# Kernel tuning notes

Hardware: AMD Instinct MI355X
Metric: run time of the kernel (lower is better)

Reference implementation:

```python
import jax, jax.numpy as jnp
import numpy as np

B, S, D, H = 2, 2048, 1024, 16
DK = D // H  # 64
THETA = 10000.0


def _rope_tables(seq_len, d_k, theta):
    pos = jnp.arange(seq_len, dtype=jnp.float32)  # [S]
    dim = jnp.arange(0, d_k, 2, dtype=jnp.float32)  # [DK/2]
    inv_freq = 1.0 / theta ** (dim / d_k)
    angle = pos[:, None] * inv_freq[None, :]  # [S, DK/2]
    angle = jnp.repeat(angle, 2, axis=-1)  # repeat_interleave -> [S, DK]
    return jnp.cos(angle), jnp.sin(angle)


def _apply_rope(x, cos, sin):
    # x: [..., S, DK]; interleaved pair rotation
    x1 = x[..., ::2]
    x2 = x[..., 1::2]
    x_perm = jnp.stack([-x2, x1], axis=-1).reshape(x.shape)
    return x * cos + x_perm * sin


def setup_inputs() -> dict:
    key = jax.random.key(0)
    ks = jax.random.split(key, 5)
    std = np.sqrt(2.0 / (D + D)).astype(np.float32)
    return {
        "x": jax.random.normal(ks[0], (B, S, D), dtype=jnp.float32),
        "Wq": jax.random.normal(ks[1], (D, D), dtype=jnp.float32) * std,
        "Wk": jax.random.normal(ks[2], (D, D), dtype=jnp.float32) * std,
        "Wv": jax.random.normal(ks[3], (D, D), dtype=jnp.float32) * std,
        "Wo": jax.random.normal(ks[4], (D, D), dtype=jnp.float32) * std,
    }


def reference(x, Wq, Wk, Wv, Wo):
    seq_len = x.shape[-2]
    # projections: weight is [d_out, d_in], applied as x @ W^T
    def split_heads(t):
        return t.reshape(*t.shape[:-1], H, DK).swapaxes(-3, -2)  # [B, H, S, DK]

    Q = split_heads(jnp.einsum('bsd,od->bso', x, Wq))
    K = split_heads(jnp.einsum('bsd,od->bso', x, Wk))
    V = split_heads(jnp.einsum('bsd,od->bso', x, Wv))

    cos, sin = _rope_tables(seq_len, DK, THETA)  # [S, DK]
    Q = _apply_rope(Q, cos, sin)
    K = _apply_rope(K, cos, sin)

    scale = 1.0 / np.sqrt(DK).astype(np.float32)
    logits = jnp.einsum('bhnd,bhmd->bhnm', Q, K) * scale  # [B, H, S, S]
    causal = jnp.tril(jnp.ones((seq_len, seq_len), dtype=bool))
    logits = jnp.where(causal, logits, -jnp.inf)
    probs = jax.nn.softmax(logits, axis=-1)
    attn = jnp.einsum('bhnm,bhmd->bhnd', probs, V)  # [B, H, S, DK]
    attn = attn.swapaxes(-3, -2).reshape(*x.shape[:-1], D)  # [B, S, D]
    return jnp.einsum('bsd,od->bso', attn, Wo)
```

## Files before the change

### kernel.cpp

```cpp
#include <hip/hip_runtime.h>
#include <hip/hip_bf16.h>
#include <cstdint>
#include <cstddef>

#define BB 2
#define SS 2048
#define DD 1024
#define HH 16
#define DKK 64
#define MM (BB*SS)

typedef __bf16 bf16x8 __attribute__((ext_vector_type(8)));
typedef float  f32x4  __attribute__((ext_vector_type(4)));

__device__ __forceinline__ unsigned short f2bf(float f) {
    unsigned u = __float_as_uint(f);
    u += 0x7FFF + ((u >> 16) & 1);
    return (unsigned short)(u >> 16);
}

#if __has_builtin(__builtin_amdgcn_cvt_pk_bf16_f32)
typedef __bf16 bf16v2 __attribute__((ext_vector_type(2)));
__device__ __forceinline__ unsigned pk_bf16(float a, float b) {
    bf16v2 v = __builtin_amdgcn_cvt_pk_bf16_f32(a, b);
    return __builtin_bit_cast(unsigned, v);
}
#else
__device__ __forceinline__ unsigned pk_bf16(float a, float b) {
    return (unsigned)f2bf(a) | ((unsigned)f2bf(b) << 16);
}
#endif

__device__ __forceinline__ void gld_lds16(const void* g, void* l) {
    __builtin_amdgcn_global_load_lds(
        (const __attribute__((address_space(1))) unsigned int*)g,
        (__attribute__((address_space(3))) unsigned int*)l, 16, 0, 0);
}

#define WAIT_VM4() __builtin_amdgcn_s_waitcnt(0x0F74)
#define WAIT_VM3() __builtin_amdgcn_s_waitcnt(0x0F73)
#define WAIT_VM0() __builtin_amdgcn_s_waitcnt(0x0F70)
#define BARRIER()  __builtin_amdgcn_s_barrier()

__global__ __launch_bounds__(256) void cast_all(const float* __restrict__ x,
                                                const float* __restrict__ wq,
                                                const float* __restrict__ wk,
                                                const float* __restrict__ wv,
                                                const float* __restrict__ wo,
                                                unsigned short* __restrict__ xb,
                                                unsigned short* __restrict__ wb) {
    int i = (blockIdx.x * 256 + threadIdx.x) * 4;
    const float* src;
    unsigned short* dst;
    if (i < MM * DD) { src = x + i; dst = xb + i; }
    else {
        int e = i - MM * DD;
        int r = e >> 20;
        const float* s0 = (r == 0) ? wq : (r == 1) ? wk : (r == 2) ? wv : wo;
        src = s0 + (e & ((1 << 20) - 1));
        dst = wb + e;
    }
    float4 v = *reinterpret_cast<const float4*>(src);
    ushort4 o;
    o.x = f2bf(v.x); o.y = f2bf(v.y); o.z = f2bf(v.z); o.w = f2bf(v.w);
    *reinterpret_cast<ushort4*>(dst) = o;
}

__global__ __launch_bounds__(256, 3) void gemm_qkv(const unsigned short* __restrict__ A,
                                                   const unsigned short* __restrict__ W,
                                                   unsigned short* __restrict__ Qo,
                                                   unsigned short* __restrict__ Ko,
                                                   unsigned short* __restrict__ Vto) {
    __shared__ __align__(16) unsigned short A0[128 * 32], W0[128 * 32];
    __shared__ __align__(16) unsigned short A1[128 * 32], W1[128 * 32];
    const int tid  = threadIdx.x;
    const int wave = tid >> 6, lane = tid & 63;
    const int quad = lane >> 4, l16 = lane & 15;
    const int wm = wave >> 1, wn = wave & 1;
    const int m0 = blockIdx.y * 128, n0 = blockIdx.x * 128;
    const int sw3 = l16 & 3;

    f32x4 acc[4][4];
    for (int i = 0; i < 4; i++)
        for (int j = 0; j < 4; j++) acc[i][j] = f32x4{0.f, 0.f, 0.f, 0.f};

    auto stage = [&](int k0, unsigned short* As, unsigned short* Ws) {
        for (int c = tid; c < 512; c += 256) {
            int row = c >> 2, g = c & 3;
            int gc = ((g ^ (row & 3)) << 3);
            gld_lds16(A + (size_t)(m0 + row) * DD + k0 + gc, As + c * 8);
            gld_lds16(W + (size_t)(n0 + row) * DD + k0 + gc, Ws + c * 8);
        }
    };
    auto compute = [&](const unsigned short* As, const unsigned short* Ws) {
        bf16x8 af[4], bfb[4];
        for (int i = 0; i < 4; i++)
            af[i] = *reinterpret_cast<const bf16x8*>(As + (wm * 64 + i * 16 + l16) * 32 + ((quad ^ sw3) << 3));
        for (int j = 0; j < 4; j++)
            bfb[j] = *reinterpret_cast<const bf16x8*>(Ws + (wn * 64 + j * 16 + l16) * 32 + ((quad ^ sw3) << 3));
        for (int i = 0; i < 4; i++)
            for (int j = 0; j < 4; j++)
                acc[i][j] = __builtin_amdgcn_mfma_f32_16x16x32_bf16(af[i], bfb[j], acc[i][j], 0, 0, 0);
    };

    stage(0, A0, W0);
    int k0 = 0;
    while (true) {
        BARRIER();
        if (k0 + 32 < DD) { stage(k0 + 32, A1, W1); WAIT_VM4(); } else WAIT_VM0();
        BARRIER();
        compute(A0, W0);
        k0 += 32; if (k0 >= DD) break;

        BARRIER();
        if (k0 + 32 < DD) { stage(k0 + 32, A0, W0); WAIT_VM4(); } else WAIT_VM0();
        BARRIER();
        compute(A1, W1);
        k0 += 32; if (k0 >= DD) break;
    }

    const int region = n0 >> 10;
    const float L2T_OVER_DK = 13.287712379549449f / 64.0f;
    if (region < 2) {
        __syncthreads();
        float* T = (float*)A0 + wave * 512;
        unsigned short* Co = region ? Ko : Qo;
        const int sl  = lane >> 2;
        const int dkl = (lane & 3) * 4;
        for (int i = 0; i < 4; i++) {
            int ms0 = m0 + wm * 64 + i * 16;
            int b = ms0 >> 11;
            int s = (ms0 & 2047) + sl;
            for (int j = 0; j < 4; j++) {
                int nc = (n0 + wn * 64 + j * 16) & 1023;
                int h = nc >> 6;
                int dk0 = (nc & 63) + dkl;
                for (int r = 0; r < 4; r++)
                    T[(quad * 4 + r) * 20 + l16] = acc[i][j][r];
                float4 v4 = *reinterpret_cast<const float4*>(T + sl * 20 + dkl);
                float if0 = exp2f(-(float)(dk0)     * L2T_OVER_DK);
                float if1 = exp2f(-(float)(dk0 + 2) * L2T_OVER_DK);
                float sn0, cs0, sn1, cs1;
                __sincosf((float)s * if0, &sn0, &cs0);
                __sincosf((float)s * if1, &sn1, &cs1);
                float e0 = v4.x * cs0 - v4.y * sn0;
                float o0 = v4.y * cs0 + v4.x * sn0;
                float e1 = v4.z * cs1 - v4.w * sn1;
                float o1 = v4.w * cs1 + v4.z * sn1;
                uint2 st;
                st.x = pk_bf16(e0, o0);
                st.y = pk_bf16(e1, o1);
                *reinterpret_cast<uint2*>(Co + ((size_t)(b * HH + h) * SS + s) * DKK + dk0) = st;
            }
        }
    } else {
        __syncthreads();
        unsigned short* T = A0 + wave * 1024;
        const int dkl = lane >> 2, s4 = (lane & 3) * 4;
        for (int i = 0; i < 4; i++) {
            int ms0 = m0 + wm * 64 + i * 16;
            for (int j = 0; j < 4; j++) {
                int nc0 = n0 + wn * 64 + j * 16;
                for (int r = 0; r < 4; r++)
                    T[(quad * 4 + r) * 17 + l16] = f2bf(acc[i][j][r]);
                ushort4 o;
                o.x = T[(s4 + 0) * 17 + dkl];
                o.y = T[(s4 + 1) * 17 + dkl];
                o.z = T[(s4 + 2) * 17 + dkl];
                o.w = T[(s4 + 3) * 17 + dkl];
                int nc = (nc0 + dkl) & 1023;
                int h = nc >> 6, dk = nc & 63;
                int m = ms0 + s4;
                int b = m >> 11, s = m & 2047;
                *reinterpret_cast<ushort4*>(Vto + ((size_t)((b * HH + h) * DKK + dk)) * SS + s) = o;
            }
        }
    }
}

__global__ __launch_bounds__(256, 3) void gemm_out(const unsigned short* __restrict__ A,
                                                   const unsigned short* __restrict__ W,
                                                   float* __restrict__ C) {
    __shared__ __align__(16) unsigned short A0[64 * 32], W0[128 * 32];
    __shared__ __align__(16) unsigned short A1[64 * 32], W1[128 * 32];
    const int tid  = threadIdx.x;
    const int wave = tid >> 6, lane = tid & 63;
    const int quad = lane >> 4, l16 = lane & 15;
    const int wm = wave >> 1, wn = wave & 1;
    const int m0 = blockIdx.y * 64, n0 = blockIdx.x * 128;
    const int sw3 = l16 & 3;

    f32x4 acc[2][4];
    for (int i = 0; i < 2; i++)
        for (int j = 0; j < 4; j++) acc[i][j] = f32x4{0.f, 0.f, 0.f, 0.f};

    auto stage = [&](int k0, unsigned short* As, unsigned short* Ws) {
        {
            int row = tid >> 2, g = tid & 3;
            int gc = ((g ^ (row & 3)) << 3);
            gld_lds16(A + (size_t)(m0 + row) * DD + k0 + gc, As + tid * 8);
        }
        for (int c = tid; c < 512; c += 256) {
            int row = c >> 2, g = c & 3;
            int gc = ((g ^ (row & 3)) << 3);
            gld_lds16(W + (size_t)(n0 + row) * DD + k0 + gc, Ws + c * 8);
        }
    };
    auto compute = [&](const unsigned short* As, const unsigned short* Ws) {
        bf16x8 af[2], bfb[4];
        for (int i = 0; i < 2; i++)
            af[i] = *reinterpret_cast<const bf16x8*>(As + (wm * 32 + i * 16 + l16) * 32 + ((quad ^ sw3) << 3));
        for (int j = 0; j < 4; j++)
            bfb[j] = *reinterpret_cast<const bf16x8*>(Ws + (wn * 64 + j * 16 + l16) * 32 + ((quad ^ sw3) << 3));
        for (int i = 0; i < 2; i++)
            for (int j = 0; j < 4; j++)
                acc[i][j] = __builtin_amdgcn_mfma_f32_16x16x32_bf16(af[i], bfb[j], acc[i][j], 0, 0, 0);
    };

    stage(0, A0, W0);
    int k0 = 0;
    while (true) {
        BARRIER();
        if (k0 + 32 < DD) { stage(k0 + 32, A1, W1); WAIT_VM3(); } else WAIT_VM0();
        BARRIER();
        compute(A0, W0);
        k0 += 32; if (k0 >= DD) break;

        BARRIER();
        if (k0 + 32 < DD) { stage(k0 + 32, A0, W0); WAIT_VM3(); } else WAIT_VM0();
        BARRIER();
        compute(A1, W1);
        k0 += 32; if (k0 >= DD) break;
    }

    for (int i = 0; i < 2; i++) {
        int mrow = m0 + wm * 32 + i * 16 + quad * 4;
        for (int j = 0; j < 4; j++) {
            int ncol = n0 + wn * 64 + j * 16 + l16;
            for (int r = 0; r < 4; r++)
                C[(size_t)(mrow + r) * DD + ncol] = acc[i][j][r];
        }
    }
}

__global__ __launch_bounds__(256) void attn_kernel(const unsigned short* __restrict__ Qb,
                                                   const unsigned short* __restrict__ Kb,
                                                   const unsigned short* __restrict__ Vtb,
                                                   unsigned short* __restrict__ attn) {
    __shared__ unsigned short K0s[64 * 64], V0s[64 * 64];
    __shared__ unsigned short K1s[64 * 64], V1s[64 * 64];
    __shared__ unsigned short Ps[4][16 * 72];

    const int tid  = threadIdx.x;
    const int wave = tid >> 6, lane = tid & 63;
    const int quad = lane >> 4, l16 = lane & 15;
    const int t  = blockIdx.x;
    const int bh = blockIdx.y;
    const int sw = l16 & 7;
    const int qlo = t * 64, qhi = (31 - t) * 64;
    const int nIter = 32 - t;

    const unsigned short* Qg = Qb  + (size_t)bh * SS * DKK;
    const unsigned short* Kg = Kb  + (size_t)bh * SS * DKK;
    const unsigned short* Vg = Vtb + (size_t)bh * DKK * SS;

    bf16x8 qL0 = *reinterpret_cast<const bf16x8*>(Qg + (size_t)(qlo + wave * 16 + l16) * DKK + quad * 8);
    bf16x8 qL1 = *reinterpret_cast<const bf16x8*>(Qg + (size_t)(qlo + wave * 16 + l16) * DKK + 32 + quad * 8);
    bf16x8 qH0 = *reinterpret_cast<const bf16x8*>(Qg + (size_t)(qhi + wave * 16 + l16) * DKK + quad * 8);
    bf16x8 qH1 = *reinterpret_cast<const bf16x8*>(Qg + (size_t)(qhi + wave * 16 + l16) * DKK + 32 + quad * 8);

    bf16x8 vone;
    for (int tt = 0; tt < 8; tt++) vone[tt] = (__bf16)1.0f;

    f32x4 aoL[4], aoH[4], alL, alH;
    for (int j = 0; j < 4; j++) { aoL[j] = f32x4{0.f,0.f,0.f,0.f}; aoH[j] = f32x4{0.f,0.f,0.f,0.f}; }
    alL = f32x4{0.f,0.f,0.f,0.f}; alH = f32x4{0.f,0.f,0.f,0.f};

    auto stage = [&](int it, unsigned short* Kd, unsigned short* Vd) {
        const int kv0 = it * 64;
        for (int c = tid; c < 512; c += 256) {
            int row = c >> 3, g = c & 7;
            int gc = ((g ^ (row & 7)) << 3);
            gld_lds16(Kg + (size_t)(kv0 + row) * DKK + gc, Kd + c * 8);
            gld_lds16(Vg + (size_t)row * SS + kv0 + gc, Vd + c * 8);
        }
    };

    const float C1 = 0.18033688011112042f;
    const float NB = -11.541560327111707f;

    auto do_tile = [&](const unsigned short* Kd, const unsigned short* Vd,
                       bf16x8 q0f, bf16x8 q1f, bool diag,
                       f32x4* ao, f32x4& al) {
        f32x4 sc[4];
        for (int j = 0; j < 4; j++) {
            const unsigned short* kr = Kd + (j * 16 + l16) * 64;
            bf16x8 kf0 = *reinterpret_cast<const bf16x8*>(kr + ((quad ^ sw) << 3));
            bf16x8 kf1 = *reinterpret_cast<const bf16x8*>(kr + (((4 + quad) ^ sw) << 3));
            f32x4 s = f32x4{0.f, 0.f, 0.f, 0.f};
            s = __builtin_amdgcn_mfma_f32_16x16x32_bf16(q0f, kf0, s, 0, 0, 0);
            s = __builtin_amdgcn_mfma_f32_16x16x32_bf16(q1f, kf1, s, 0, 0, 0);
            sc[j] = s;
        }
        if (diag) {
            for (int j = 0; j < 4; j++) {
                int lcol = j * 16 + l16;
                for (int r = 0; r < 4; r++) {
                    int lrow = wave * 16 + quad * 4 + r;
                    if (lcol > lrow) sc[j][r] = -1e30f;
                }
            }
        }
        for (int j = 0; j < 4; j++)
            for (int r = 0; r < 4; r++)
                sc[j][r] = exp2f(fmaf(sc[j][r], C1, NB));

        unsigned short* Pw = Ps[wave];
        for (int r = 0; r < 4; r++) {
            unsigned pA = pk_bf16(sc[0][r], sc[1][r]);
            unsigned pB = pk_bf16(sc[2][r], sc[3][r]);
            int ro = (quad * 4 + r) * 72;
            Pw[ro + l16]      = (unsigned short)pA;
            Pw[ro + 16 + l16] = (unsigned short)(pA >> 16);
            Pw[ro + 32 + l16] = (unsigned short)pB;
            Pw[ro + 48 + l16] = (unsigned short)(pB >> 16);
        }

        for (int ko = 0; ko < 64; ko += 32) {
            bf16x8 pf = *reinterpret_cast<const bf16x8*>(Pw + l16 * 72 + ko + quad * 8);
            al = __builtin_amdgcn_mfma_f32_16x16x32_bf16(pf, vone, al, 0, 0, 0);
            int gh = (ko >> 3) + quad;
            for (int j = 0; j < 4; j++) {
                bf16x8 vf = *reinterpret_cast<const bf16x8*>(Vd + (j * 16 + l16) * 64 + ((gh ^ sw) << 3));
                ao[j] = __builtin_amdgcn_mfma_f32_16x16x32_bf16(pf, vf, ao[j], 0, 0, 0);
            }
        }
    };

    stage(0, K0s, V0s);
    int it = 0;
    while (true) {
        BARRIER();
        if (it + 1 < nIter) { stage(it + 1, K1s, V1s); WAIT_VM4(); } else WAIT_VM0();
        BARRIER();
        do_tile(K0s, V0s, qH0, qH1, it == nIter - 1, aoH, alH);
        if (it <= t) do_tile(K0s, V0s, qL0, qL1, it == t, aoL, alL);
        if (++it >= nIter) break;

        BARRIER();
        if (it + 1 < nIter) { stage(it + 1, K0s, V0s); WAIT_VM4(); } else WAIT_VM0();
        BARRIER();
        do_tile(K1s, V1s, qH0, qH1, it == nIter - 1, aoH, alH);
        if (it <= t) do_tile(K1s, V1s, qL0, qL1, it == t, aoL, alL);
        if (++it >= nIter) break;
    }

    const int b = bh >> 4, h = bh & 15;
    for (int r = 0; r < 4; r++) {
        float invL = __builtin_amdgcn_rcpf(alL[r]);
        float invH = __builtin_amdgcn_rcpf(alH[r]);
        int srL = qlo + wave * 16 + quad * 4 + r;
        int srH = qhi + wave * 16 + quad * 4 + r;
        for (int j = 0; j < 4; j++) {
            attn[((size_t)(b * SS + srL)) * DD + h * DKK + j * 16 + l16] = f2bf(aoL[j][r] * invL);
            attn[((size_t)(b * SS + srH)) * DD + h * DKK + j * 16 + l16] = f2bf(aoH[j][r] * invH);
        }
    }
}

extern "C" void kernel_launch(void* const* d_in, const int* in_sizes, int n_in,
                              void* d_out, int out_size, void* d_ws, size_t ws_size,
                              hipStream_t stream) {
    const float* x  = (const float*)d_in[0];
    const float* Wq = (const float*)d_in[1];
    const float* Wk = (const float*)d_in[2];
    const float* Wv = (const float*)d_in[3];
    const float* Wo = (const float*)d_in[4];

    char* ws = (char*)d_ws;
    const size_t MB = 1u << 20;
    unsigned short* xb    = (unsigned short*)(ws);
    unsigned short* wb    = (unsigned short*)(ws + 8  * MB);
    unsigned short* Qbuf  = (unsigned short*)(ws + 16 * MB);
    unsigned short* Kbuf  = (unsigned short*)(ws + 24 * MB);
    unsigned short* Vtbuf = (unsigned short*)(ws + 32 * MB);
    unsigned short* attnb = xb;

    cast_all<<<8192, 256, 0, stream>>>(x, Wq, Wk, Wv, Wo, xb, wb);

    gemm_qkv<<<dim3(24, 32), 256, 0, stream>>>(xb, wb, Qbuf, Kbuf, Vtbuf);

    attn_kernel<<<dim3(16, BB * HH), 256, 0, stream>>>(Qbuf, Kbuf, Vtbuf, attnb);

    gemm_out<<<dim3(8, 64), 256, 0, stream>>>(attnb, wb + 3 * 1024 * 1024, (float*)d_out);
}
```

Measured before the change: 190.4 us.

## Stage 128-key KV tiles in attention and shuffle-based RoPE epilogue

The attention kernel now stages 128 keys per pipeline stage, processed as two 64-key sub-tiles, so it needs half as many barriers and waitcnt stalls. The V tile layout gets a wider 16-way XOR swizzle. The QKV GEMM epilogue drops its LDS transpose and instead pairs RoPE elements with a lane xor-shuffle, writing scalar bf16 stores. The risks are doubled LDS use per block, which may lower occupancy, and narrower, less coalesced global stores in the epilogue.

```diff
diff --git a/kernel.cpp b/kernel.cpp
--- a/kernel.cpp
+++ b/kernel.cpp
@@ -37,6 +37,7 @@
         (__attribute__((address_space(3))) unsigned int*)l, 16, 0, 0);
 }
 
+#define WAIT_VM8() __builtin_amdgcn_s_waitcnt(0x0F78)
 #define WAIT_VM4() __builtin_amdgcn_s_waitcnt(0x0F74)
 #define WAIT_VM3() __builtin_amdgcn_s_waitcnt(0x0F73)
 #define WAIT_VM0() __builtin_amdgcn_s_waitcnt(0x0F70)
@@ -122,35 +123,22 @@
     const int region = n0 >> 10;
     const float L2T_OVER_DK = 13.287712379549449f / 64.0f;
     if (region < 2) {
-        __syncthreads();
-        float* T = (float*)A0 + wave * 512;
         unsigned short* Co = region ? Ko : Qo;
-        const int sl  = lane >> 2;
-        const int dkl = (lane & 3) * 4;
         for (int i = 0; i < 4; i++) {
-            int ms0 = m0 + wm * 64 + i * 16;
-            int b = ms0 >> 11;
-            int s = (ms0 & 2047) + sl;
+            int mrow = m0 + wm * 64 + i * 16 + quad * 4;
+            int b = mrow >> 11, s0 = mrow & 2047;
             for (int j = 0; j < 4; j++) {
-                int nc = (n0 + wn * 64 + j * 16) & 1023;
-                int h = nc >> 6;
-                int dk0 = (nc & 63) + dkl;
-                for (int r = 0; r < 4; r++)
-                    T[(quad * 4 + r) * 20 + l16] = acc[i][j][r];
-                float4 v4 = *reinterpret_cast<const float4*>(T + sl * 20 + dkl);
-                float if0 = exp2f(-(float)(dk0)     * L2T_OVER_DK);
-                float if1 = exp2f(-(float)(dk0 + 2) * L2T_OVER_DK);
-                float sn0, cs0, sn1, cs1;
-                __sincosf((float)s * if0, &sn0, &cs0);
-                __sincosf((float)s * if1, &sn1, &cs1);
-                float e0 = v4.x * cs0 - v4.y * sn0;
-                float o0 = v4.y * cs0 + v4.x * sn0;
-                float e1 = v4.z * cs1 - v4.w * sn1;
-                float o1 = v4.w * cs1 + v4.z * sn1;
-                uint2 st;
-                st.x = pk_bf16(e0, o0);
-                st.y = pk_bf16(e1, o1);
-                *reinterpret_cast<uint2*>(Co + ((size_t)(b * HH + h) * SS + s) * DKK + dk0) = st;
+                int nc = (n0 + wn * 64 + j * 16 + l16) & 1023;
+                int h = nc >> 6, dk = nc & 63;
+                float inv_freq = exp2f(-(float)(dk & ~1) * L2T_OVER_DK);
+                for (int r = 0; r < 4; r++) {
+                    float v = acc[i][j][r];
+                    float partner = __shfl_xor(v, 1, 64);
+                    float sn, cs;
+                    __sincosf((float)(s0 + r) * inv_freq, &sn, &cs);
+                    float outv = v * cs + ((dk & 1) ? partner : -partner) * sn;
+                    Co[((size_t)(b * HH + h) * SS + (s0 + r)) * DKK + dk] = f2bf(outv);
+                }
             }
         }
     } else {
@@ -247,8 +235,8 @@
                                                    const unsigned short* __restrict__ Kb,
                                                    const unsigned short* __restrict__ Vtb,
                                                    unsigned short* __restrict__ attn) {
-    __shared__ unsigned short K0s[64 * 64], V0s[64 * 64];
-    __shared__ unsigned short K1s[64 * 64], V1s[64 * 64];
+    __shared__ unsigned short K0s[128 * 64], V0s[64 * 128];
+    __shared__ unsigned short K1s[128 * 64], V1s[64 * 128];
     __shared__ unsigned short Ps[4][16 * 72];
 
     const int tid  = threadIdx.x;
@@ -256,9 +244,10 @@
     const int quad = lane >> 4, l16 = lane & 15;
     const int t  = blockIdx.x;
     const int bh = blockIdx.y;
-    const int sw = l16 & 7;
+    const int swK = l16 & 7;
     const int qlo = t * 64, qhi = (31 - t) * 64;
     const int nIter = 32 - t;
+    const int nStage = (nIter + 1) >> 1;
 
     const unsigned short* Qg = Qb  + (size_t)bh * SS * DKK;
     const unsigned short* Kg = Kb  + (size_t)bh * SS * DKK;
@@ -276,27 +265,27 @@
     for (int j = 0; j < 4; j++) { aoL[j] = f32x4{0.f,0.f,0.f,0.f}; aoH[j] = f32x4{0.f,0.f,0.f,0.f}; }
     alL = f32x4{0.f,0.f,0.f,0.f}; alH = f32x4{0.f,0.f,0.f,0.f};
 
-    auto stage = [&](int it, unsigned short* Kd, unsigned short* Vd) {
-        const int kv0 = it * 64;
-        for (int c = tid; c < 512; c += 256) {
-            int row = c >> 3, g = c & 7;
-            int gc = ((g ^ (row & 7)) << 3);
-            gld_lds16(Kg + (size_t)(kv0 + row) * DKK + gc, Kd + c * 8);
-            gld_lds16(Vg + (size_t)row * SS + kv0 + gc, Vd + c * 8);
+    auto stage = [&](int s2, unsigned short* Kd, unsigned short* Vd) {
+        const int kv0 = s2 * 128;
+        for (int c = tid; c < 1024; c += 256) {
+            int rowK = c >> 3, gK = c & 7;
+            gld_lds16(Kg + (size_t)(kv0 + rowK) * DKK + ((gK ^ (rowK & 7)) << 3), Kd + c * 8);
+            int rowV = c >> 4, gV = c & 15;
+            gld_lds16(Vg + (size_t)rowV * SS + kv0 + ((gV ^ (rowV & 15)) << 3), Vd + c * 8);
         }
     };
 
     const float C1 = 0.18033688011112042f;
     const float NB = -11.541560327111707f;
 
-    auto do_tile = [&](const unsigned short* Kd, const unsigned short* Vd,
+    auto do_tile = [&](const unsigned short* Kd, const unsigned short* Vd, int sub,
                        bf16x8 q0f, bf16x8 q1f, bool diag,
                        f32x4* ao, f32x4& al) {
         f32x4 sc[4];
         for (int j = 0; j < 4; j++) {
-            const unsigned short* kr = Kd + (j * 16 + l16) * 64;
-            bf16x8 kf0 = *reinterpret_cast<const bf16x8*>(kr + ((quad ^ sw) << 3));
-            bf16x8 kf1 = *reinterpret_cast<const bf16x8*>(kr + (((4 + quad) ^ sw) << 3));
+            const unsigned short* kr = Kd + (sub * 64 + j * 16 + l16) * 64;
+            bf16x8 kf0 = *reinterpret_cast<const bf16x8*>(kr + ((quad ^ swK) << 3));
+            bf16x8 kf1 = *reinterpret_cast<const bf16x8*>(kr + (((4 + quad) ^ swK) << 3));
             f32x4 s = f32x4{0.f, 0.f, 0.f, 0.f};
             s = __builtin_amdgcn_mfma_f32_16x16x32_bf16(q0f, kf0, s, 0, 0, 0);
             s = __builtin_amdgcn_mfma_f32_16x16x32_bf16(q1f, kf1, s, 0, 0, 0);
@@ -329,30 +318,37 @@
         for (int ko = 0; ko < 64; ko += 32) {
             bf16x8 pf = *reinterpret_cast<const bf16x8*>(Pw + l16 * 72 + ko + quad * 8);
             al = __builtin_amdgcn_mfma_f32_16x16x32_bf16(pf, vone, al, 0, 0, 0);
-            int gh = (ko >> 3) + quad;
+            int gg = sub * 8 + (ko >> 3) + quad;
             for (int j = 0; j < 4; j++) {
-                bf16x8 vf = *reinterpret_cast<const bf16x8*>(Vd + (j * 16 + l16) * 64 + ((gh ^ sw) << 3));
+                bf16x8 vf = *reinterpret_cast<const bf16x8*>(Vd + (j * 16 + l16) * 128 + ((gg ^ l16) << 3));
                 ao[j] = __builtin_amdgcn_mfma_f32_16x16x32_bf16(pf, vf, ao[j], 0, 0, 0);
             }
         }
     };
 
+    auto process = [&](const unsigned short* Kd, const unsigned short* Vd, int s2) {
+        for (int sub = 0; sub < 2; sub++) {
+            int idx = 2 * s2 + sub;
+            if (idx >= nIter) break;
+            do_tile(Kd, Vd, sub, qH0, qH1, idx == nIter - 1, aoH, alH);
+            if (idx <= t) do_tile(Kd, Vd, sub, qL0, qL1, idx == t, aoL, alL);
+        }
+    };
+
     stage(0, K0s, V0s);
-    int it = 0;
+    int s2 = 0;
     while (true) {
         BARRIER();
-        if (it + 1 < nIter) { stage(it + 1, K1s, V1s); WAIT_VM4(); } else WAIT_VM0();
-        BARRIER();
-        do_tile(K0s, V0s, qH0, qH1, it == nIter - 1, aoH, alH);
-        if (it <= t) do_tile(K0s, V0s, qL0, qL1, it == t, aoL, alL);
-        if (++it >= nIter) break;
-
-        BARRIER();
-        if (it + 1 < nIter) { stage(it + 1, K0s, V0s); WAIT_VM4(); } else WAIT_VM0();
-        BARRIER();
-        do_tile(K1s, V1s, qH0, qH1, it == nIter - 1, aoH, alH);
-        if (it <= t) do_tile(K1s, V1s, qL0, qL1, it == t, aoL, alL);
-        if (++it >= nIter) break;
+        if (s2 + 1 < nStage) { stage(s2 + 1, K1s, V1s); WAIT_VM8(); } else WAIT_VM0();
+        BARRIER();
+        process(K0s, V0s, s2);
+        if (++s2 >= nStage) break;
+
+        BARRIER();
+        if (s2 + 1 < nStage) { stage(s2 + 1, K0s, V0s); WAIT_VM8(); } else WAIT_VM0();
+        BARRIER();
+        process(K1s, V1s, s2);
+        if (++s2 >= nStage) break;
     }
 
     const int b = bh >> 4, h = bh & 15;
```

New measurement: 182.0 us. 1.05x faster.
